# Kernel tuning notes

Hardware: AMD Instinct MI355X
Metric: run time of the kernel (lower is better)

The kernel has to match this reference:

```python
import jax, jax.numpy as jnp
import numpy as np

N_NODES = 150000
N_ETYPES = 1000
B = 16384
D_CONT = 2
N_NCAT = 3
NCAT_CARD = 64
NCAT_DIM = 16
ETYPE_DIM = 32
N_ECAT = 2
ECAT_CARD = 32
ECAT_DIM = 16
T_DIM = 16
D_IN = D_CONT + N_NCAT * NCAT_DIM      # 50
H = 128                                 # gnn_hidden_dim
P_IN = 2 * H + ETYPE_DIM + N_ECAT * ECAT_DIM + T_DIM  # 336
P_HID = 64


def setup_inputs() -> dict:
    key = jax.random.key(0)
    ks = jax.random.split(key, 24)
    s = 0.05
    inp = {
        "src_node_ids": jax.random.randint(ks[0], (B,), 0, N_NODES),
        "dst_node_ids": jax.random.randint(ks[1], (B,), 0, N_NODES),
        "edge_type_ids": jax.random.randint(ks[2], (B,), 0, N_ETYPES),
        "t_rel": jax.random.uniform(ks[3], (B, 1), dtype=jnp.float32),
        "node_cont": jax.random.normal(ks[4], (N_NODES, D_CONT), dtype=jnp.float32),
        "node_cat_codes": jax.random.randint(ks[5], (N_NCAT, N_NODES), 0, NCAT_CARD),
        "edge_cat_codes": jax.random.randint(ks[6], (N_ECAT, N_ETYPES), 0, ECAT_CARD),
        "edge_index": jax.random.randint(ks[7], (2, 1500000), 0, N_NODES),
        "h_prev": jax.random.normal(ks[8], (N_NODES, H), dtype=jnp.float32),
        "c_prev": jax.random.normal(ks[9], (N_NODES, H), dtype=jnp.float32),
        # learned parameters
        "node_cat_emb": jax.random.normal(ks[10], (N_NCAT, NCAT_CARD, NCAT_DIM), dtype=jnp.float32) * s,
        "edge_id_emb": jax.random.normal(ks[11], (N_ETYPES, ETYPE_DIM), dtype=jnp.float32) * s,
        "edge_cat_emb": jax.random.normal(ks[12], (N_ECAT, ECAT_CARD, ECAT_DIM), dtype=jnp.float32) * s,
        "time_W": jax.random.normal(ks[13], (1, T_DIM), dtype=jnp.float32) * s,
        "time_b": jnp.zeros((T_DIM,), dtype=jnp.float32),
        # GConvLSTM (ChebConv K=1 per gate): gates ordered [i, f, c, o]
        "Wx": jax.random.normal(ks[14], (4, D_IN, H), dtype=jnp.float32) * s,
        "Wh": jax.random.normal(ks[15], (4, H, H), dtype=jnp.float32) * s,
        "b_gate": jnp.zeros((4, H), dtype=jnp.float32),
        "w_c": jax.random.normal(ks[16], (3, H), dtype=jnp.float32) * s,  # peephole for i, f, o
        "W1": jax.random.normal(ks[17], (P_IN, P_HID), dtype=jnp.float32) * s,
        "b1": jnp.zeros((P_HID,), dtype=jnp.float32),
        "W2": jax.random.normal(ks[18], (P_HID, 1), dtype=jnp.float32) * s,
        "b2": jnp.zeros((1,), dtype=jnp.float32),
    }
    return inp


def reference(src_node_ids, dst_node_ids, edge_type_ids, t_rel, node_cont,
              node_cat_codes, edge_cat_codes, edge_index, h_prev, c_prev,
              node_cat_emb, edge_id_emb, edge_cat_emb, time_W, time_b,
              Wx, Wh, b_gate, w_c, W1, b1, W2, b2):
    # --- process node features: cont + 3 categorical embedding gathers ---
    # node_cat_emb[f, node_cat_codes[f, n]] -> [N_NCAT, N, NCAT_DIM]
    cat_e = node_cat_emb[jnp.arange(N_NCAT)[:, None], node_cat_codes]
    cat_e = jnp.transpose(cat_e, (1, 0, 2)).reshape(N_NODES, N_NCAT * NCAT_DIM)
    x = jnp.concatenate([node_cont, cat_e], axis=-1)  # [N, D_IN]

    # --- process batch edge-type features ---
    eid_e = edge_id_emb[edge_type_ids]                               # [B, 32]
    codes_b = edge_cat_codes[:, edge_type_ids]                       # [N_ECAT, B]
    ecat_e = edge_cat_emb[jnp.arange(N_ECAT)[:, None], codes_b]      # [N_ECAT, B, 16]
    ecat_e = jnp.transpose(ecat_e, (1, 0, 2)).reshape(-1, N_ECAT * ECAT_DIM)
    edge_feat = jnp.concatenate([eid_e, ecat_e], axis=-1)            # [B, 64]

    # --- time encoding ---
    t = t_rel if t_rel.ndim == 2 else t_rel[:, None]
    time_e = t @ time_W + time_b                                     # [B, 16]

    # --- GConvLSTM step. ChebConv with K=1: out = x @ W0 + b (T_0(L)x = x),
    # so edge_index is mathematically unused. Gates: [i, f, c_tilde, o]. ---
    z = (jnp.einsum('nd,gdh->gnh', x, Wx)
         + jnp.einsum('nh,ghk->gnk', h_prev, Wh)
         + b_gate[:, None, :])                                       # [4, N, H]
    i_g = jax.nn.sigmoid(z[0] + w_c[0] * c_prev)
    f_g = jax.nn.sigmoid(z[1] + w_c[1] * c_prev)
    t_g = jnp.tanh(z[2])
    c_new = f_g * c_prev + i_g * t_g
    o_g = jax.nn.sigmoid(z[3] + w_c[2] * c_new)
    h_new = o_g * jnp.tanh(c_new)

    # --- link predictor ---
    src_e = h_new[src_node_ids]                                      # [B, H]
    dst_e = h_new[dst_node_ids]                                      # [B, H]
    comb = jnp.concatenate([src_e, dst_e, edge_feat, time_e], axis=-1)  # [B, 336]
    hid = jax.nn.relu(comb @ W1 + b1)
    prob = jax.nn.sigmoid(hid @ W2 + b2)[:, 0]                       # [B]
    return prob, h_new, c_new
```

## Files before the change

kernel.cpp:

```cpp
#include <hip/hip_runtime.h>

#define N_NODES   150000
#define N_PAD     150016
#define B_EDGES   16384
#define H         128
#define KP        192
#define N_NCAT    3
#define NCAT_CARD 64
#define NCAT_DIM  16
#define N_ETYPES  1000
#define ETYPE_DIM 32
#define N_ECAT    2
#define ECAT_CARD 32
#define ECAT_DIM  16
#define T_DIM     16
#define P_IN      336
#define P_HID     64

typedef __bf16 bf16x8 __attribute__((ext_vector_type(8)));
typedef float  f32x4  __attribute__((ext_vector_type(4)));

__device__ __forceinline__ float sigmoidf_(float x) { return 1.0f / (1.0f + __expf(-x)); }
__device__ __forceinline__ float tanhf_(float x)    { return 1.0f - 2.0f / (__expf(2.0f * x) + 1.0f); }
__device__ __forceinline__ unsigned short f2bf(float f) {
    unsigned u = __float_as_uint(f);
    u += 0x7fffu + ((u >> 16) & 1u);
    return (unsigned short)(u >> 16);
}
__device__ __forceinline__ void async_copy16(const void* g, void* l) {
    __builtin_amdgcn_global_load_lds(
        (const __attribute__((address_space(1))) unsigned int*)g,
        (__attribute__((address_space(3))) unsigned int*)l, 16, 0, 0);
}

__global__ __launch_bounds__(256) void build_a_kernel(
    const float* __restrict__ node_cont,
    const int*   __restrict__ node_cat_codes,
    const float* __restrict__ node_cat_emb,
    const float* __restrict__ h_prev,
    unsigned short* __restrict__ A)
{
    const int t = threadIdx.x;
    const int r = t >> 5, l32 = t & 31;
    const int n = blockIdx.x * 8 + r;
    if (n >= N_PAD) return;
    unsigned short* arow = A + (size_t)n * KP;
    #pragma unroll
    for (int s = 0; s < 6; ++s) {
        int j = s * 32 + l32;
        float v = 0.0f;
        if (n < N_NODES) {
            if (j < 2) {
                v = node_cont[n * 2 + j];
            } else if (j < 50) {
                int c = (j - 2) >> 4, d = (j - 2) & 15;
                int code = node_cat_codes[c * N_NODES + n];
                v = node_cat_emb[(c * NCAT_CARD + code) * NCAT_DIM + d];
            } else if (j < 178) {
                v = h_prev[n * H + (j - 50)];
            }
        }
        arow[j] = f2bf(v);
    }
}

__global__ __launch_bounds__(192) void build_w_kernel(
    const float* __restrict__ Wx, const float* __restrict__ Wh,
    unsigned short* __restrict__ Wt)
{
    const int c = blockIdx.x, k = threadIdx.x;
    const int h = c >> 2, g = c & 3;
    float v = 0.0f;
    if (k < 50)       v = Wx[(g * 50 + k) * H + h];
    else if (k < 178) v = Wh[(g * H + (k - 50)) * H + h];
    Wt[c * KP + k] = f2bf(v);
}

__global__ __launch_bounds__(256) void lstm_mfma_kernel(
    const unsigned short* __restrict__ A,
    const unsigned short* __restrict__ Wt,
    const float* __restrict__ c_prev,
    const float* __restrict__ b_gate,
    const float* __restrict__ w_c,
    float* __restrict__ h_out,
    float* __restrict__ c_out)
{
    __shared__ __align__(16) unsigned short Asub[128 * 32];
    __shared__ __align__(16) unsigned short Wsub[128 * 32];
    __shared__ float zbuf[64 * 132];

    const int t    = threadIdx.x;
    const int wv   = t >> 6, ln = t & 63;
    const int wm   = wv >> 1, wn = wv & 1;
    const int quad = ln >> 4, m16 = ln & 15;
    const int bx   = blockIdx.x, by = blockIdx.y;

    f32x4 acc[4][4];
    #pragma unroll
    for (int i = 0; i < 4; ++i)
        #pragma unroll
        for (int j = 0; j < 4; ++j) acc[i][j] = (f32x4){0.f, 0.f, 0.f, 0.f};

    const unsigned short* Ablk = A  + (size_t)(bx * 128) * KP;
    const unsigned short* Wblk = Wt + (size_t)(by * 128) * KP;

    for (int kc = 0; kc < 6; ++kc) {
        #pragma unroll
        for (int i = 0; i < 2; ++i) {
            int slot = wv * 128 + i * 64 + ln;
            int r = slot >> 2, sl = slot & 3;
            int s = sl ^ ((r >> 1) & 3);
            const unsigned short* ga = Ablk + (size_t)r * KP + kc * 32 + s * 8;
            const unsigned short* gw = Wblk + (size_t)r * KP + kc * 32 + s * 8;
            char* la = (char*)Asub + (wv * 128 + i * 64) * 16;
            char* lw = (char*)Wsub + (wv * 128 + i * 64) * 16;
            async_copy16(ga, la);
            async_copy16(gw, lw);
        }
        __syncthreads();

        bf16x8 af[4], bf[4];
        #pragma unroll
        for (int mi = 0; mi < 4; ++mi) {
            int r = wm * 64 + mi * 16 + m16;
            int atom = quad ^ ((r >> 1) & 3);
            af[mi] = *(const bf16x8*)(Asub + r * 32 + atom * 8);
        }
        #pragma unroll
        for (int ni = 0; ni < 4; ++ni) {
            int r = wn * 64 + ni * 16 + m16;
            int atom = quad ^ ((r >> 1) & 3);
            bf[ni] = *(const bf16x8*)(Wsub + r * 32 + atom * 8);
        }
        #pragma unroll
        for (int mi = 0; mi < 4; ++mi)
            #pragma unroll
            for (int ni = 0; ni < 4; ++ni)
                acc[mi][ni] = __builtin_amdgcn_mfma_f32_16x16x32_bf16(
                    af[mi], bf[ni], acc[mi][ni], 0, 0, 0);
        __syncthreads();
    }

    #pragma unroll
    for (int half = 0; half < 2; ++half) {
        if (wm == half) {
            #pragma unroll
            for (int mi = 0; mi < 4; ++mi)
                #pragma unroll
                for (int ni = 0; ni < 4; ++ni)
                    #pragma unroll
                    for (int r = 0; r < 4; ++r)
                        zbuf[(mi * 16 + quad * 4 + r) * 132 + wn * 64 + ni * 16 + m16]
                            = acc[mi][ni][r];
        }
        __syncthreads();
        #pragma unroll
        for (int p = 0; p < 8; ++p) {
            int idx = t + p * 256;
            int row = idx >> 5, hl = idx & 31;
            int node = bx * 128 + half * 64 + row;
            int hg = by * 32 + hl;
            if (node < N_NODES) {
                float z0 = zbuf[row * 132 + hl * 4 + 0] + b_gate[0 * H + hg];
                float z1 = zbuf[row * 132 + hl * 4 + 1] + b_gate[1 * H + hg];
                float z2 = zbuf[row * 132 + hl * 4 + 2] + b_gate[2 * H + hg];
                float z3 = zbuf[row * 132 + hl * 4 + 3] + b_gate[3 * H + hg];
                float cp = c_prev[(size_t)node * H + hg];
                float ig = sigmoidf_(z0 + w_c[0 * H + hg] * cp);
                float fg = sigmoidf_(z1 + w_c[1 * H + hg] * cp);
                float tg = tanhf_(z2);
                float cn = fg * cp + ig * tg;
                float og = sigmoidf_(z3 + w_c[2 * H + hg] * cn);
                h_out[(size_t)node * H + hg] = og * tanhf_(cn);
                c_out[(size_t)node * H + hg] = cn;
            }
        }
        __syncthreads();
    }
}

__global__ __launch_bounds__(256) void edge_kernel(
    const int*   __restrict__ src,
    const int*   __restrict__ dst,
    const int*   __restrict__ et,
    const float* __restrict__ t_rel,
    const int*   __restrict__ edge_cat_codes,
    const float* __restrict__ edge_id_emb,
    const float* __restrict__ edge_cat_emb,
    const float* __restrict__ time_W,
    const float* __restrict__ time_b,
    const float* __restrict__ W1,
    const float* __restrict__ b1,
    const float* __restrict__ W2,
    const float* __restrict__ b2,
    const float* __restrict__ h_new,
    float* __restrict__ prob)
{
    __shared__ __align__(16) float comb[4][P_IN];
    const int t = threadIdx.x;
    const int el = t >> 6;
    const int j  = t & 63;
    const int e  = blockIdx.x * 4 + el;

    if (e < B_EDGES) {
        const int s = src[e], d = dst[e], ety = et[e];
        comb[el][j]       = h_new[(size_t)s * H + j];
        comb[el][64 + j]  = h_new[(size_t)s * H + 64 + j];
        comb[el][128 + j] = h_new[(size_t)d * H + j];
        comb[el][192 + j] = h_new[(size_t)d * H + 64 + j];
        if (j < 32) {
            comb[el][256 + j] = edge_id_emb[ety * ETYPE_DIM + j];
            int c = j >> 4, dd = j & 15;
            int code = edge_cat_codes[c * N_ETYPES + ety];
            comb[el][288 + j] = edge_cat_emb[(c * ECAT_CARD + code) * ECAT_DIM + dd];
        }
        if (j < T_DIM) comb[el][320 + j] = t_rel[e] * time_W[j] + time_b[j];
    }
    __syncthreads();
    if (e >= B_EDGES) return;

    float h0 = b1[j], h1 = 0.f, h2 = 0.f, h3 = 0.f;
    #pragma unroll 4
    for (int k = 0; k < P_IN; k += 4) {
        float4 cv = *(const float4*)&comb[el][k];
        h0 = fmaf(cv.x, W1[(k + 0) * P_HID + j], h0);
        h1 = fmaf(cv.y, W1[(k + 1) * P_HID + j], h1);
        h2 = fmaf(cv.z, W1[(k + 2) * P_HID + j], h2);
        h3 = fmaf(cv.w, W1[(k + 3) * P_HID + j], h3);
    }
    float hid = fmaxf((h0 + h1) + (h2 + h3), 0.0f);

    float v = hid * W2[j];
    #pragma unroll
    for (int off = 32; off > 0; off >>= 1) v += __shfl_down(v, off);
    if (j == 0) prob[e] = sigmoidf_(v + b2[0]);
}

extern "C" void kernel_launch(void* const* d_in, const int* in_sizes, int n_in,
                              void* d_out, int out_size, void* d_ws, size_t ws_size,
                              hipStream_t stream) {
    const int*   src            = (const int*)  d_in[0];
    const int*   dst            = (const int*)  d_in[1];
    const int*   et             = (const int*)  d_in[2];
    const float* t_rel          = (const float*)d_in[3];
    const float* node_cont      = (const float*)d_in[4];
    const int*   node_cat_codes = (const int*)  d_in[5];
    const int*   edge_cat_codes = (const int*)  d_in[6];
    const float* h_prev         = (const float*)d_in[8];
    const float* c_prev         = (const float*)d_in[9];
    const float* node_cat_emb   = (const float*)d_in[10];
    const float* edge_id_emb    = (const float*)d_in[11];
    const float* edge_cat_emb   = (const float*)d_in[12];
    const float* time_W         = (const float*)d_in[13];
    const float* time_b         = (const float*)d_in[14];
    const float* Wx             = (const float*)d_in[15];
    const float* Wh             = (const float*)d_in[16];
    const float* b_gate         = (const float*)d_in[17];
    const float* w_c            = (const float*)d_in[18];
    const float* W1             = (const float*)d_in[19];
    const float* b1             = (const float*)d_in[20];
    const float* W2             = (const float*)d_in[21];
    const float* b2             = (const float*)d_in[22];

    float* out   = (float*)d_out;
    float* prob  = out;
    float* h_out = out + B_EDGES;
    float* c_out = out + B_EDGES + (size_t)N_NODES * H;

    unsigned short* A  = (unsigned short*)d_ws;
    unsigned short* Wt = (unsigned short*)((char*)d_ws + (size_t)N_PAD * KP * 2);

    build_a_kernel<<<N_PAD / 8, 256, 0, stream>>>(node_cont, node_cat_codes,
                                                  node_cat_emb, h_prev, A);
    build_w_kernel<<<512, 192, 0, stream>>>(Wx, Wh, Wt);

    dim3 grid(N_PAD / 128, 4);
    lstm_mfma_kernel<<<grid, 256, 0, stream>>>(A, Wt, c_prev, b_gate, w_c,
                                               h_out, c_out);

    edge_kernel<<<B_EDGES / 4, 256, 0, stream>>>(src, dst, et, t_rel,
                                                 edge_cat_codes, edge_id_emb, edge_cat_emb,
                                                 time_W, time_b, W1, b1, W2, b2,
                                                 h_out, prob);
}
```

Baseline: 533.7 us.

## Reorder gate weight columns so LSTM epilogue runs from MFMA registers without LDS

Permutes the transposed gate-weight layout so each wave's four 16-column MFMA tiles hold the i, f, c, o gates for the same 16 hidden units. The LSTM kernel can then apply the cell update straight from accumulators, with no shared-memory staging. Operands are loaded directly from global memory instead of async copies into swizzled LDS, and the grid becomes 2 column blocks by 64-node tiles. c_prev is prefetched before the GEMM, and hardware reciprocal replaces division in sigmoid and tanh. This removes barriers and LDS traffic, but global loads are now strided and uncoalesced, and A rows are reread by both column blocks.

```diff
diff --git a/kernel.cpp b/kernel.cpp
--- a/kernel.cpp
+++ b/kernel.cpp
@@ -20,17 +20,13 @@
 typedef __bf16 bf16x8 __attribute__((ext_vector_type(8)));
 typedef float  f32x4  __attribute__((ext_vector_type(4)));
 
-__device__ __forceinline__ float sigmoidf_(float x) { return 1.0f / (1.0f + __expf(-x)); }
-__device__ __forceinline__ float tanhf_(float x)    { return 1.0f - 2.0f / (__expf(2.0f * x) + 1.0f); }
+__device__ __forceinline__ float rcp_(float x)      { return __builtin_amdgcn_rcpf(x); }
+__device__ __forceinline__ float sigmoidf_(float x) { return rcp_(1.0f + __expf(-x)); }
+__device__ __forceinline__ float tanhf_(float x)    { return 1.0f - 2.0f * rcp_(__expf(2.0f * x) + 1.0f); }
 __device__ __forceinline__ unsigned short f2bf(float f) {
     unsigned u = __float_as_uint(f);
     u += 0x7fffu + ((u >> 16) & 1u);
     return (unsigned short)(u >> 16);
-}
-__device__ __forceinline__ void async_copy16(const void* g, void* l) {
-    __builtin_amdgcn_global_load_lds(
-        (const __attribute__((address_space(1))) unsigned int*)g,
-        (__attribute__((address_space(3))) unsigned int*)l, 16, 0, 0);
 }
 
 __global__ __launch_bounds__(256) void build_a_kernel(
@@ -69,7 +65,11 @@
     unsigned short* __restrict__ Wt)
 {
     const int c = blockIdx.x, k = threadIdx.x;
-    const int h = c >> 2, g = c & 3;
+    const int m16 = c & 15;
+    const int g   = (c >> 4) & 3;
+    const int w   = (c >> 6) & 3;
+    const int cbh = c >> 8;
+    const int h   = cbh * 64 + w * 16 + m16;
     float v = 0.0f;
     if (k < 50)       v = Wx[(g * 50 + k) * H + h];
     else if (k < 178) v = Wh[(g * H + (k - 50)) * H + h];
@@ -85,15 +85,32 @@
     float* __restrict__ h_out,
     float* __restrict__ c_out)
 {
-    __shared__ __align__(16) unsigned short Asub[128 * 32];
-    __shared__ __align__(16) unsigned short Wsub[128 * 32];
-    __shared__ float zbuf[64 * 132];
-
     const int t    = threadIdx.x;
     const int wv   = t >> 6, ln = t & 63;
-    const int wm   = wv >> 1, wn = wv & 1;
     const int quad = ln >> 4, m16 = ln & 15;
-    const int bx   = blockIdx.x, by = blockIdx.y;
+    const int cb   = blockIdx.x;
+    const int nb   = blockIdx.y;
+    const int nbase = nb * 64;
+    const int h     = cb * 64 + wv * 16 + m16;
+
+    const unsigned short* aptr[4];
+    const unsigned short* wptr[4];
+    #pragma unroll
+    for (int mi = 0; mi < 4; ++mi)
+        aptr[mi] = A + (size_t)(nbase + mi * 16 + m16) * KP + quad * 8;
+    const int cwave = cb * 256 + wv * 64;
+    #pragma unroll
+    for (int ni = 0; ni < 4; ++ni)
+        wptr[ni] = Wt + (size_t)(cwave + ni * 16 + m16) * KP + quad * 8;
+
+    float cpv[4][4];
+    #pragma unroll
+    for (int mi = 0; mi < 4; ++mi)
+        #pragma unroll
+        for (int r = 0; r < 4; ++r) {
+            int node = nbase + mi * 16 + quad * 4 + r;
+            cpv[mi][r] = (node < N_NODES) ? c_prev[(size_t)node * H + h] : 0.0f;
+        }
 
     f32x4 acc[4][4];
     #pragma unroll
@@ -101,82 +118,44 @@
         #pragma unroll
         for (int j = 0; j < 4; ++j) acc[i][j] = (f32x4){0.f, 0.f, 0.f, 0.f};
 
-    const unsigned short* Ablk = A  + (size_t)(bx * 128) * KP;
-    const unsigned short* Wblk = Wt + (size_t)(by * 128) * KP;
-
+    #pragma unroll
     for (int kc = 0; kc < 6; ++kc) {
-        #pragma unroll
-        for (int i = 0; i < 2; ++i) {
-            int slot = wv * 128 + i * 64 + ln;
-            int r = slot >> 2, sl = slot & 3;
-            int s = sl ^ ((r >> 1) & 3);
-            const unsigned short* ga = Ablk + (size_t)r * KP + kc * 32 + s * 8;
-            const unsigned short* gw = Wblk + (size_t)r * KP + kc * 32 + s * 8;
-            char* la = (char*)Asub + (wv * 128 + i * 64) * 16;
-            char* lw = (char*)Wsub + (wv * 128 + i * 64) * 16;
-            async_copy16(ga, la);
-            async_copy16(gw, lw);
-        }
-        __syncthreads();
-
         bf16x8 af[4], bf[4];
         #pragma unroll
-        for (int mi = 0; mi < 4; ++mi) {
-            int r = wm * 64 + mi * 16 + m16;
-            int atom = quad ^ ((r >> 1) & 3);
-            af[mi] = *(const bf16x8*)(Asub + r * 32 + atom * 8);
-        }
-        #pragma unroll
-        for (int ni = 0; ni < 4; ++ni) {
-            int r = wn * 64 + ni * 16 + m16;
-            int atom = quad ^ ((r >> 1) & 3);
-            bf[ni] = *(const bf16x8*)(Wsub + r * 32 + atom * 8);
-        }
+        for (int mi = 0; mi < 4; ++mi)
+            af[mi] = *(const bf16x8*)(aptr[mi] + kc * 32);
+        #pragma unroll
+        for (int ni = 0; ni < 4; ++ni)
+            bf[ni] = *(const bf16x8*)(wptr[ni] + kc * 32);
         #pragma unroll
         for (int mi = 0; mi < 4; ++mi)
             #pragma unroll
             for (int ni = 0; ni < 4; ++ni)
                 acc[mi][ni] = __builtin_amdgcn_mfma_f32_16x16x32_bf16(
                     af[mi], bf[ni], acc[mi][ni], 0, 0, 0);
-        __syncthreads();
-    }
-
-    #pragma unroll
-    for (int half = 0; half < 2; ++half) {
-        if (wm == half) {
-            #pragma unroll
-            for (int mi = 0; mi < 4; ++mi)
-                #pragma unroll
-                for (int ni = 0; ni < 4; ++ni)
-                    #pragma unroll
-                    for (int r = 0; r < 4; ++r)
-                        zbuf[(mi * 16 + quad * 4 + r) * 132 + wn * 64 + ni * 16 + m16]
-                            = acc[mi][ni][r];
-        }
-        __syncthreads();
-        #pragma unroll
-        for (int p = 0; p < 8; ++p) {
-            int idx = t + p * 256;
-            int row = idx >> 5, hl = idx & 31;
-            int node = bx * 128 + half * 64 + row;
-            int hg = by * 32 + hl;
+    }
+
+    const float bg0 = b_gate[0 * H + h], bg1 = b_gate[1 * H + h];
+    const float bg2 = b_gate[2 * H + h], bg3 = b_gate[3 * H + h];
+    const float wc0 = w_c[0 * H + h], wc1 = w_c[1 * H + h], wc2 = w_c[2 * H + h];
+
+    #pragma unroll
+    for (int mi = 0; mi < 4; ++mi)
+        #pragma unroll
+        for (int r = 0; r < 4; ++r) {
+            int node = nbase + mi * 16 + quad * 4 + r;
             if (node < N_NODES) {
-                float z0 = zbuf[row * 132 + hl * 4 + 0] + b_gate[0 * H + hg];
-                float z1 = zbuf[row * 132 + hl * 4 + 1] + b_gate[1 * H + hg];
-                float z2 = zbuf[row * 132 + hl * 4 + 2] + b_gate[2 * H + hg];
-                float z3 = zbuf[row * 132 + hl * 4 + 3] + b_gate[3 * H + hg];
-                float cp = c_prev[(size_t)node * H + hg];
-                float ig = sigmoidf_(z0 + w_c[0 * H + hg] * cp);
-                float fg = sigmoidf_(z1 + w_c[1 * H + hg] * cp);
-                float tg = tanhf_(z2);
+                size_t off = (size_t)node * H + h;
+                float cp = cpv[mi][r];
+                float ig = sigmoidf_(acc[mi][0][r] + bg0 + wc0 * cp);
+                float fg = sigmoidf_(acc[mi][1][r] + bg1 + wc1 * cp);
+                float tg = tanhf_(acc[mi][2][r] + bg2);
                 float cn = fg * cp + ig * tg;
-                float og = sigmoidf_(z3 + w_c[2 * H + hg] * cn);
-                h_out[(size_t)node * H + hg] = og * tanhf_(cn);
-                c_out[(size_t)node * H + hg] = cn;
+                float og = sigmoidf_(acc[mi][3][r] + bg3 + wc2 * cn);
+                h_out[off] = og * tanhf_(cn);
+                c_out[off] = cn;
             }
         }
-        __syncthreads();
-    }
 }
 
 __global__ __launch_bounds__(256) void edge_kernel(
@@ -274,7 +253,7 @@
                                                   node_cat_emb, h_prev, A);
     build_w_kernel<<<512, 192, 0, stream>>>(Wx, Wh, Wt);
 
-    dim3 grid(N_PAD / 128, 4);
+    dim3 grid(2, N_PAD / 64);
     lstm_mfma_kernel<<<grid, 256, 0, stream>>>(A, Wt, c_prev, b_gate, w_c,
                                                h_out, c_out);
 
```

Result: faster. 517.9 us (-3.0%).
